# Kernel tuning notes

Measured on AMD Instinct MI355X. Metric: run time of the kernel, lower is better.

## Reference

```python
import jax, jax.numpy as jnp
import numpy as np

EPS = 1e-6
NEG_SLOPE = 0.2


def setup_inputs() -> dict:
    key = jax.random.key(0)
    k1, k2 = jax.random.split(key)
    B, D, T = 4, 512, 2048
    H, Dh = 8, 512 // 8
    x = jax.random.normal(k1, (B, D, T), dtype=jnp.float32)
    qkv = jax.random.normal(k2, (3, H, D, Dh), dtype=jnp.float32) * 0.02
    norm_w = jnp.ones((1,), dtype=jnp.float32)
    return {"x": x, "qkv": qkv, "norm_w": norm_w}


def reference(x, qkv, norm_w):
    B, D, T = x.shape
    H = qkv.shape[1]
    # leaky relu on channels-first input
    x = jnp.where(x >= 0, x, NEG_SLOPE * x)
    # fused QKV projection: (B,D,T),(3,H,D,Dh) -> (3,B,H,T,Dh)
    h = jnp.einsum('bdt,nhdD->nbhtD', x, qkv)
    # RMSNorm over the sequence axis (dim=-2), scalar learned weight
    denom = jnp.mean(h * h, axis=-2, keepdims=True)
    h = norm_w * (h / jnp.sqrt(denom + EPS))
    q, k, v = h[0], h[1], h[2]
    scale = jnp.sqrt(jnp.asarray(D // H, dtype=x.dtype))
    # manual attention: (B,H,T,T) score matrix
    attn = jax.nn.softmax(jnp.einsum('bhtD,bhTD->bhtT', q, k) / scale, axis=-1)
    # weighted values, output laid out (B,H,Dh,T) then merged to (B,D,T)
    out = jnp.einsum('bhtT,bhTD->bhDt', attn, v)
    return out.reshape(B, D, T)
```

## Files before the change

### kernel.cpp

```cpp
#include <hip/hip_runtime.h>
#include <cstddef>

#define B   4
#define D   512
#define T   2048
#define H   8
#define DH  64
#define NEG_SLOPE 0.2f
#define EPS 1e-6f
#define LOG2E 1.44269504088896340736f

typedef __attribute__((ext_vector_type(8))) short short8;
typedef __attribute__((ext_vector_type(4))) float float4v;

__device__ __forceinline__ float bf2f(ushort u) {
    unsigned int x = ((unsigned int)u) << 16;
    return __builtin_bit_cast(float, x);
}
__device__ __forceinline__ ushort f2bf(float f) {
    unsigned int x = __builtin_bit_cast(unsigned int, f);
    x = x + 0x7fffu + ((x >> 16) & 1u);
    return (ushort)(x >> 16);
}

__global__ __launch_bounds__(256) void transpose_lrelu(const float* __restrict__ src,
                                                       ushort* __restrict__ dst,
                                                       int src_ld, int dst_ld,
                                                       size_t src_mstride, size_t dst_mstride,
                                                       int do_lrelu,
                                                       float* __restrict__ zbuf, int zcount) {
    const int tid = threadIdx.x;
    if (zbuf != nullptr && blockIdx.x == 0 && blockIdx.y == 0 && blockIdx.z == 0) {
        for (int i = tid; i < zcount; i += 256) zbuf[i] = 0.f;
    }

    const int c0 = blockIdx.x * 64, r0 = blockIdx.y * 64;
    const float* s = src + blockIdx.z * src_mstride + (size_t)r0 * src_ld + c0;
    ushort*      d = dst + blockIdx.z * dst_mstride + (size_t)c0 * dst_ld + r0;

    __shared__ float Ls[64][68];

    const int rl = tid >> 4, c4 = (tid & 15) * 4;
    #pragma unroll
    for (int p = 0; p < 4; ++p) {
        float4 v = *(const float4*)(s + (size_t)(rl + p * 16) * src_ld + c4);
        if (do_lrelu) {
            v.x = fmaxf(v.x, NEG_SLOPE * v.x);
            v.y = fmaxf(v.y, NEG_SLOPE * v.y);
            v.z = fmaxf(v.z, NEG_SLOPE * v.z);
            v.w = fmaxf(v.w, NEG_SLOPE * v.w);
        }
        *(float4*)&Ls[rl + p * 16][c4] = v;
    }
    __syncthreads();

    const int tl = tid >> 2;
    #pragma unroll
    for (int it = 0; it < 2; ++it) {
        int ch = (tid & 3) + it * 4;
        ushort o[8];
        #pragma unroll
        for (int j = 0; j < 8; ++j) o[j] = f2bf(Ls[ch * 8 + j][tl]);
        *(uint4*)(d + (size_t)tl * dst_ld + ch * 8) = *(uint4*)o;
    }
}

__global__ __launch_bounds__(256) void qkv_mm(const ushort* __restrict__ xT,
                                              const ushort* __restrict__ WT,
                                              ushort* __restrict__ hb,
                                              ushort* __restrict__ vT,
                                              float* __restrict__ ssq) {
    const int tid = threadIdx.x, wave = tid >> 6, lane = tid & 63;
    const int quad = lane >> 4, l16 = lane & 15;
    const int wr = wave >> 1, wc = wave & 1;
    const int t0  = blockIdx.x * 128;
    const int gd0 = blockIdx.y * 128;
    const int b   = blockIdx.z;

    __shared__ ushort At[128 * 64];
    __shared__ ushort Bt[128 * 64];

    const ushort* xb = xT + (size_t)b * T * D + (size_t)t0 * D;
    const ushort* wb = WT + (size_t)gd0 * D;

    const int srow = lane >> 3;
    const int csrc = (lane & 7) ^ srow;

    float4v acc[4][4];
    #pragma unroll
    for (int i = 0; i < 4; ++i)
        #pragma unroll
        for (int j = 0; j < 4; ++j) acc[i][j] = (float4v){0.f, 0.f, 0.f, 0.f};

    for (int k0 = 0; k0 < D; k0 += 64) {
        #pragma unroll
        for (int i = 0; i < 4; ++i) {
            int rbase = wave * 32 + i * 8;
            int row = rbase + srow;
            const ushort* ga = xb + (size_t)row * D + k0 + csrc * 8;
            const ushort* gb = wb + (size_t)row * D + k0 + csrc * 8;
            __builtin_amdgcn_global_load_lds(
                (const __attribute__((address_space(1))) unsigned int*)ga,
                (__attribute__((address_space(3))) unsigned int*)&At[rbase * 64], 16, 0, 0);
            __builtin_amdgcn_global_load_lds(
                (const __attribute__((address_space(1))) unsigned int*)gb,
                (__attribute__((address_space(3))) unsigned int*)&Bt[rbase * 64], 16, 0, 0);
        }
        __syncthreads();

        #pragma unroll
        for (int kh = 0; kh < 2; ++kh) {
            short8 aF[4], bF[4];
            #pragma unroll
            for (int mt = 0; mt < 4; ++mt) {
                int row = wr * 64 + mt * 16 + l16;
                aF[mt] = *(const short8*)&At[row * 64 + (((kh * 4 + quad) ^ (l16 & 7)) * 8)];
            }
            #pragma unroll
            for (int nt = 0; nt < 4; ++nt) {
                int row = wc * 64 + nt * 16 + l16;
                bF[nt] = *(const short8*)&Bt[row * 64 + (((kh * 4 + quad) ^ (l16 & 7)) * 8)];
            }
            #pragma unroll
            for (int mt = 0; mt < 4; ++mt)
                #pragma unroll
                for (int nt = 0; nt < 4; ++nt)
                    acc[mt][nt] = __builtin_amdgcn_mfma_f32_16x16x32_bf16(
                        aF[mt], bF[nt], acc[mt][nt], 0, 0, 0);
        }
        __syncthreads();
    }

    const int g = blockIdx.y * 2 + wc;
    const int n = g >> 3, hh = g & 7;
    float colsq[4] = {0.f, 0.f, 0.f, 0.f};

    if (n < 2) {
        ushort* hbase = hb + (((size_t)n * B + b) * H + hh) * (size_t)T * DH;
        #pragma unroll
        for (int mt = 0; mt < 4; ++mt) {
            #pragma unroll
            for (int nt = 0; nt < 4; ++nt) {
                float4v c = acc[mt][nt];
                int dd = nt * 16 + l16;
                #pragma unroll
                for (int r = 0; r < 4; ++r) {
                    int t = t0 + wr * 64 + mt * 16 + quad * 4 + r;
                    hbase[(size_t)t * DH + dd] = f2bf(c[r]);
                    colsq[nt] += c[r] * c[r];
                }
            }
        }
    } else {
        ushort* vbase = vT + ((size_t)b * H + hh) * (size_t)DH * T;
        #pragma unroll
        for (int mt = 0; mt < 4; ++mt) {
            #pragma unroll
            for (int nt = 0; nt < 4; ++nt) {
                float4v c = acc[mt][nt];
                int dd = nt * 16 + l16;
                int t  = t0 + wr * 64 + mt * 16 + quad * 4;
                ushort4 pk;
                pk.x = f2bf(c[0]); pk.y = f2bf(c[1]);
                pk.z = f2bf(c[2]); pk.w = f2bf(c[3]);
                *(ushort4*)(vbase + (size_t)dd * T + t) = pk;
                colsq[nt] += c[0]*c[0] + c[1]*c[1] + c[2]*c[2] + c[3]*c[3];
            }
        }
    }
    #pragma unroll
    for (int nt = 0; nt < 4; ++nt) {
        float s = colsq[nt];
        s += __shfl_xor(s, 16);
        s += __shfl_xor(s, 32);
        if (quad == 0)
            atomicAdd(&ssq[(((size_t)n * B + b) * H + hh) * 64 + nt * 16 + l16], s);
    }
}

__global__ __launch_bounds__(256, 4) void flash_attn(const ushort* __restrict__ hb,
                                                     const ushort* __restrict__ vT,
                                                     const float* __restrict__ ssq,
                                                     const float* __restrict__ norm_w,
                                                     float* __restrict__ out) {
    const int tid  = threadIdx.x;
    const int wave = tid >> 6;
    const int lane = tid & 63;
    const int quad = lane >> 4;
    const int l16  = lane & 15;

    const int lin  = blockIdx.x;
    const int head = ((lin & 7) << 2) | ((lin >> 3) & 3);
    const int t0   = (lin >> 5) * 64;
    const int b    = head >> 3, hh = head & 7;

    const size_t slab = (size_t)B * H * T * DH;
    const ushort* qp = hb + (size_t)head * T * DH;
    const ushort* kp = hb + slab + (size_t)head * T * DH;
    const ushort* vp = vT + (size_t)head * DH * T;

    __shared__ ushort Kt[64 * 64];
    __shared__ ushort Vt[64 * 64];
    __shared__ ushort Pb[4][16 * 64];
    __shared__ float fqk[64], sv[64];

    if (tid < 64) {
        float nw = norm_w[0];
        float mq = ssq[(0 * B * H + head) * 64 + tid] * (1.0f / T) + EPS;
        float mk = ssq[(1 * B * H + head) * 64 + tid] * (1.0f / T) + EPS;
        float mv = ssq[(2 * B * H + head) * 64 + tid] * (1.0f / T) + EPS;
        fqk[tid] = nw * nw * rsqrtf(mq) * rsqrtf(mk) * 0.125f * LOG2E;
        sv[tid]  = nw * rsqrtf(mv);
    }
    __syncthreads();

    short8 bQ[2];
    {
        const ushort* qr = qp + (size_t)(t0 + wave * 16 + l16) * DH;
        #pragma unroll
        for (int kh = 0; kh < 2; ++kh) {
            short8 raw = *(const short8*)(qr + kh * 32 + quad * 8);
            #pragma unroll
            for (int j = 0; j < 8; ++j) {
                float f = bf2f((ushort)raw[j]) * fqk[kh * 32 + quad * 8 + j];
                bQ[kh][j] = (short)f2bf(f);
            }
        }
    }

    const int srow = lane >> 3;
    const int csrc = (lane & 7) ^ srow;
    const ushort* kA = kp + (size_t)(wave * 16 + srow) * DH + csrc * 8;
    const ushort* kB = kp + (size_t)(wave * 16 + 8 + srow) * DH + csrc * 8;
    const ushort* vA = vp + (size_t)(wave * 16 + srow) * T + csrc * 8;
    const ushort* vB = vp + (size_t)(wave * 16 + 8 + srow) * T + csrc * 8;

    float l_run = 0.f;
    float4v O[4];
    #pragma unroll
    for (int dt = 0; dt < 4; ++dt) O[dt] = (float4v){0.f, 0.f, 0.f, 0.f};

    for (int j0 = 0; j0 < T; j0 += 64) {
        __builtin_amdgcn_global_load_lds(
            (const __attribute__((address_space(1))) unsigned int*)(kA + (size_t)j0 * DH),
            (__attribute__((address_space(3))) unsigned int*)&Kt[(wave * 16) * 64], 16, 0, 0);
        __builtin_amdgcn_global_load_lds(
            (const __attribute__((address_space(1))) unsigned int*)(kB + (size_t)j0 * DH),
            (__attribute__((address_space(3))) unsigned int*)&Kt[(wave * 16 + 8) * 64], 16, 0, 0);
        __builtin_amdgcn_global_load_lds(
            (const __attribute__((address_space(1))) unsigned int*)(vA + j0),
            (__attribute__((address_space(3))) unsigned int*)&Vt[(wave * 16) * 64], 16, 0, 0);
        __builtin_amdgcn_global_load_lds(
            (const __attribute__((address_space(1))) unsigned int*)(vB + j0),
            (__attribute__((address_space(3))) unsigned int*)&Vt[(wave * 16 + 8) * 64], 16, 0, 0);
        __syncthreads();

        float4v S[4];
        #pragma unroll
        for (int mt = 0; mt < 4; ++mt) S[mt] = (float4v){0.f, 0.f, 0.f, 0.f};
        #pragma unroll
        for (int kh = 0; kh < 2; ++kh) {
            #pragma unroll
            for (int mt = 0; mt < 4; ++mt) {
                int row = mt * 16 + l16;
                short8 aK = *(const short8*)&Kt[row * 64 + (((kh * 4 + quad) ^ (l16 & 7)) * 8)];
                S[mt] = __builtin_amdgcn_mfma_f32_16x16x32_bf16(aK, bQ[kh], S[mt], 0, 0, 0);
            }
        }

        #pragma unroll
        for (int mt = 0; mt < 4; ++mt) {
            float p0 = __builtin_amdgcn_exp2f(S[mt][0]);
            float p1 = __builtin_amdgcn_exp2f(S[mt][1]);
            float p2 = __builtin_amdgcn_exp2f(S[mt][2]);
            float p3 = __builtin_amdgcn_exp2f(S[mt][3]);
            l_run += (p0 + p1) + (p2 + p3);
            unsigned int a0 = __builtin_bit_cast(unsigned int, p0) + 0x8000u;
            unsigned int a1 = __builtin_bit_cast(unsigned int, p1) + 0x8000u;
            unsigned int a2 = __builtin_bit_cast(unsigned int, p2) + 0x8000u;
            unsigned int a3 = __builtin_bit_cast(unsigned int, p3) + 0x8000u;
            uint2 pk;
            pk.x = __builtin_amdgcn_perm(a1, a0, 0x07060302u);
            pk.y = __builtin_amdgcn_perm(a3, a2, 0x07060302u);
            *(uint2*)&Pb[wave][l16 * 64 + (((mt * 2 + (quad >> 1)) ^ (l16 & 7)) * 8)
                               + (quad & 1) * 4] = pk;
        }

        #pragma unroll
        for (int kh = 0; kh < 2; ++kh) {
            short8 bP = *(const short8*)&Pb[wave][l16 * 64 + (((kh * 4 + quad) ^ (l16 & 7)) * 8)];
            #pragma unroll
            for (int dt = 0; dt < 4; ++dt) {
                int row = dt * 16 + l16;
                short8 aV = *(const short8*)&Vt[row * 64 + (((kh * 4 + quad) ^ (row & 7)) * 8)];
                O[dt] = __builtin_amdgcn_mfma_f32_16x16x32_bf16(aV, bP, O[dt], 0, 0, 0);
            }
        }
        __syncthreads();
    }

    float rs = l_run;
    rs += __shfl_xor(rs, 16);
    rs += __shfl_xor(rs, 32);
    float inv = 1.f / rs;
    const int t = t0 + wave * 16 + l16;
    #pragma unroll
    for (int dt = 0; dt < 4; ++dt) {
        #pragma unroll
        for (int r = 0; r < 4; ++r) {
            int dd = dt * 16 + quad * 4 + r;
            out[((size_t)b * D + hh * DH + dd) * T + t] = O[dt][r] * inv * sv[dd];
        }
    }
}

extern "C" void kernel_launch(void* const* d_in, const int* in_sizes, int n_in,
                              void* d_out, int out_size, void* d_ws, size_t ws_size,
                              hipStream_t stream) {
    const float* x      = (const float*)d_in[0];
    const float* qkv    = (const float*)d_in[1];
    const float* norm_w = (const float*)d_in[2];
    float* out = (float*)d_out;

    const size_t HB_BYTES = (size_t)2 * B * H * T * DH * 2;
    const size_t VT_BYTES = (size_t)B * H * DH * T * 2;
    const size_t XT_BYTES = (size_t)B * T * D * 2;
    const size_t WT_BYTES = (size_t)3 * H * DH * D * 2;
    ushort* hb  = (ushort*)d_ws;
    ushort* vT  = (ushort*)((char*)d_ws + HB_BYTES);
    ushort* xT  = (ushort*)((char*)d_ws + HB_BYTES + VT_BYTES);
    ushort* WT  = (ushort*)((char*)d_ws + HB_BYTES + VT_BYTES + XT_BYTES);
    float*  ssq = (float*)((char*)d_ws + HB_BYTES + VT_BYTES + XT_BYTES + WT_BYTES);
    const int SSQ_N = 3 * B * H * DH;

    transpose_lrelu<<<dim3(T / 64, D / 64, B), 256, 0, stream>>>(
        x, xT, T, D, (size_t)D * T, (size_t)T * D, 1, ssq, SSQ_N);
    transpose_lrelu<<<dim3(DH / 64, D / 64, 3 * H), 256, 0, stream>>>(
        qkv, WT, DH, D, (size_t)D * DH, (size_t)DH * D, 0, nullptr, 0);

    qkv_mm<<<dim3(T / 128, (3 * H * DH) / 128, B), 256, 0, stream>>>(xT, WT, hb, vT, ssq);
    flash_attn<<<dim3((T / 64) * B * H), 256, 0, stream>>>(hb, vT, ssq, norm_w, out);
}
```

Measured before the change: 155.0 us.

## Process two query groups per wave and load V fragments directly into registers

Each wave now handles 32 query rows (two 16-row groups), so the block covers 128 queries and every K tile staged in LDS and every V fragment is reused twice. V is no longer staged through LDS. Each lane reads its V MFMA operands straight from global memory into registers, which removes the Vt buffer and its LDS reads. The grid is halved and the launch bound drops to 2 blocks per CU to leave room for the doubled accumulators. The costs are more register pressure, fewer waves in flight, and uncoalesced-ish direct global V loads that the barrier no longer hides behind async LDS copies.

After: 173.1 us. 1.12x slower.

```diff
diff --git a/kernel.cpp b/kernel.cpp
--- a/kernel.cpp
+++ b/kernel.cpp
@@ -178,7 +178,7 @@
     }
 }
 
-__global__ __launch_bounds__(256, 4) void flash_attn(const ushort* __restrict__ hb,
+__global__ __launch_bounds__(256, 2) void flash_attn(const ushort* __restrict__ hb,
                                                      const ushort* __restrict__ vT,
                                                      const float* __restrict__ ssq,
                                                      const float* __restrict__ norm_w,
@@ -191,7 +191,7 @@
 
     const int lin  = blockIdx.x;
     const int head = ((lin & 7) << 2) | ((lin >> 3) & 3);
-    const int t0   = (lin >> 5) * 64;
+    const int t0   = (lin >> 5) * 128;
     const int b    = head >> 3, hh = head & 7;
 
     const size_t slab = (size_t)B * H * T * DH;
@@ -200,8 +200,7 @@
     const ushort* vp = vT + (size_t)head * DH * T;
 
     __shared__ ushort Kt[64 * 64];
-    __shared__ ushort Vt[64 * 64];
-    __shared__ ushort Pb[4][16 * 64];
+    __shared__ ushort Pb[4][2][16 * 64];
     __shared__ float fqk[64], sv[64];
 
     if (tid < 64) {
@@ -214,16 +213,17 @@
     }
     __syncthreads();
 
-    short8 bQ[2];
-    {
-        const ushort* qr = qp + (size_t)(t0 + wave * 16 + l16) * DH;
+    short8 bQ[2][2];
+    #pragma unroll
+    for (int g = 0; g < 2; ++g) {
+        const ushort* qr = qp + (size_t)(t0 + wave * 32 + g * 16 + l16) * DH;
         #pragma unroll
         for (int kh = 0; kh < 2; ++kh) {
             short8 raw = *(const short8*)(qr + kh * 32 + quad * 8);
             #pragma unroll
             for (int j = 0; j < 8; ++j) {
                 float f = bf2f((ushort)raw[j]) * fqk[kh * 32 + quad * 8 + j];
-                bQ[kh][j] = (short)f2bf(f);
+                bQ[g][kh][j] = (short)f2bf(f);
             }
         }
     }
@@ -232,13 +232,13 @@
     const int csrc = (lane & 7) ^ srow;
     const ushort* kA = kp + (size_t)(wave * 16 + srow) * DH + csrc * 8;
     const ushort* kB = kp + (size_t)(wave * 16 + 8 + srow) * DH + csrc * 8;
-    const ushort* vA = vp + (size_t)(wave * 16 + srow) * T + csrc * 8;
-    const ushort* vB = vp + (size_t)(wave * 16 + 8 + srow) * T + csrc * 8;
-
-    float l_run = 0.f;
-    float4v O[4];
-    #pragma unroll
-    for (int dt = 0; dt < 4; ++dt) O[dt] = (float4v){0.f, 0.f, 0.f, 0.f};
+
+    float l_run[2] = {0.f, 0.f};
+    float4v O[2][4];
+    #pragma unroll
+    for (int g = 0; g < 2; ++g)
+        #pragma unroll
+        for (int dt = 0; dt < 4; ++dt) O[g][dt] = (float4v){0.f, 0.f, 0.f, 0.f};
 
     for (int j0 = 0; j0 < T; j0 += 64) {
         __builtin_amdgcn_global_load_lds(
@@ -247,69 +247,88 @@
         __builtin_amdgcn_global_load_lds(
             (const __attribute__((address_space(1))) unsigned int*)(kB + (size_t)j0 * DH),
             (__attribute__((address_space(3))) unsigned int*)&Kt[(wave * 16 + 8) * 64], 16, 0, 0);
-        __builtin_amdgcn_global_load_lds(
-            (const __attribute__((address_space(1))) unsigned int*)(vA + j0),
-            (__attribute__((address_space(3))) unsigned int*)&Vt[(wave * 16) * 64], 16, 0, 0);
-        __builtin_amdgcn_global_load_lds(
-            (const __attribute__((address_space(1))) unsigned int*)(vB + j0),
-            (__attribute__((address_space(3))) unsigned int*)&Vt[(wave * 16 + 8) * 64], 16, 0, 0);
+
+        short8 aV[2][4];
+        #pragma unroll
+        for (int kh = 0; kh < 2; ++kh)
+            #pragma unroll
+            for (int dt = 0; dt < 4; ++dt)
+                aV[kh][dt] = *(const short8*)(vp + (size_t)(dt * 16 + l16) * T
+                                              + j0 + kh * 32 + quad * 8);
+
         __syncthreads();
 
-        float4v S[4];
-        #pragma unroll
-        for (int mt = 0; mt < 4; ++mt) S[mt] = (float4v){0.f, 0.f, 0.f, 0.f};
+        float4v S[2][4];
+        #pragma unroll
+        for (int g = 0; g < 2; ++g)
+            #pragma unroll
+            for (int mt = 0; mt < 4; ++mt) S[g][mt] = (float4v){0.f, 0.f, 0.f, 0.f};
         #pragma unroll
         for (int kh = 0; kh < 2; ++kh) {
+            short8 aK[4];
             #pragma unroll
             for (int mt = 0; mt < 4; ++mt) {
                 int row = mt * 16 + l16;
-                short8 aK = *(const short8*)&Kt[row * 64 + (((kh * 4 + quad) ^ (l16 & 7)) * 8)];
-                S[mt] = __builtin_amdgcn_mfma_f32_16x16x32_bf16(aK, bQ[kh], S[mt], 0, 0, 0);
-            }
-        }
-
-        #pragma unroll
-        for (int mt = 0; mt < 4; ++mt) {
-            float p0 = __builtin_amdgcn_exp2f(S[mt][0]);
-            float p1 = __builtin_amdgcn_exp2f(S[mt][1]);
-            float p2 = __builtin_amdgcn_exp2f(S[mt][2]);
-            float p3 = __builtin_amdgcn_exp2f(S[mt][3]);
-            l_run += (p0 + p1) + (p2 + p3);
-            unsigned int a0 = __builtin_bit_cast(unsigned int, p0) + 0x8000u;
-            unsigned int a1 = __builtin_bit_cast(unsigned int, p1) + 0x8000u;
-            unsigned int a2 = __builtin_bit_cast(unsigned int, p2) + 0x8000u;
-            unsigned int a3 = __builtin_bit_cast(unsigned int, p3) + 0x8000u;
-            uint2 pk;
-            pk.x = __builtin_amdgcn_perm(a1, a0, 0x07060302u);
-            pk.y = __builtin_amdgcn_perm(a3, a2, 0x07060302u);
-            *(uint2*)&Pb[wave][l16 * 64 + (((mt * 2 + (quad >> 1)) ^ (l16 & 7)) * 8)
-                               + (quad & 1) * 4] = pk;
-        }
-
-        #pragma unroll
-        for (int kh = 0; kh < 2; ++kh) {
-            short8 bP = *(const short8*)&Pb[wave][l16 * 64 + (((kh * 4 + quad) ^ (l16 & 7)) * 8)];
-            #pragma unroll
-            for (int dt = 0; dt < 4; ++dt) {
-                int row = dt * 16 + l16;
-                short8 aV = *(const short8*)&Vt[row * 64 + (((kh * 4 + quad) ^ (row & 7)) * 8)];
-                O[dt] = __builtin_amdgcn_mfma_f32_16x16x32_bf16(aV, bP, O[dt], 0, 0, 0);
-            }
-        }
+                aK[mt] = *(const short8*)&Kt[row * 64 + (((kh * 4 + quad) ^ (l16 & 7)) * 8)];
+            }
+            #pragma unroll
+            for (int g = 0; g < 2; ++g)
+                #pragma unroll
+                for (int mt = 0; mt < 4; ++mt)
+                    S[g][mt] = __builtin_amdgcn_mfma_f32_16x16x32_bf16(
+                        aK[mt], bQ[g][kh], S[g][mt], 0, 0, 0);
+        }
+
+        #pragma unroll
+        for (int g = 0; g < 2; ++g) {
+            #pragma unroll
+            for (int mt = 0; mt < 4; ++mt) {
+                float p0 = __builtin_amdgcn_exp2f(S[g][mt][0]);
+                float p1 = __builtin_amdgcn_exp2f(S[g][mt][1]);
+                float p2 = __builtin_amdgcn_exp2f(S[g][mt][2]);
+                float p3 = __builtin_amdgcn_exp2f(S[g][mt][3]);
+                l_run[g] += (p0 + p1) + (p2 + p3);
+                unsigned int a0 = __builtin_bit_cast(unsigned int, p0) + 0x8000u;
+                unsigned int a1 = __builtin_bit_cast(unsigned int, p1) + 0x8000u;
+                unsigned int a2 = __builtin_bit_cast(unsigned int, p2) + 0x8000u;
+                unsigned int a3 = __builtin_bit_cast(unsigned int, p3) + 0x8000u;
+                uint2 pk;
+                pk.x = __builtin_amdgcn_perm(a1, a0, 0x07060302u);
+                pk.y = __builtin_amdgcn_perm(a3, a2, 0x07060302u);
+                *(uint2*)&Pb[wave][g][l16 * 64 + (((mt * 2 + (quad >> 1)) ^ (l16 & 7)) * 8)
+                                      + (quad & 1) * 4] = pk;
+            }
+        }
+
+        #pragma unroll
+        for (int g = 0; g < 2; ++g) {
+            #pragma unroll
+            for (int kh = 0; kh < 2; ++kh) {
+                short8 bP = *(const short8*)&Pb[wave][g][l16 * 64 + (((kh * 4 + quad) ^ (l16 & 7)) * 8)];
+                #pragma unroll
+                for (int dt = 0; dt < 4; ++dt)
+                    O[g][dt] = __builtin_amdgcn_mfma_f32_16x16x32_bf16(
+                        aV[kh][dt], bP, O[g][dt], 0, 0, 0);
+            }
+        }
+
         __syncthreads();
     }
 
-    float rs = l_run;
-    rs += __shfl_xor(rs, 16);
-    rs += __shfl_xor(rs, 32);
-    float inv = 1.f / rs;
-    const int t = t0 + wave * 16 + l16;
-    #pragma unroll
-    for (int dt = 0; dt < 4; ++dt) {
-        #pragma unroll
-        for (int r = 0; r < 4; ++r) {
-            int dd = dt * 16 + quad * 4 + r;
-            out[((size_t)b * D + hh * DH + dd) * T + t] = O[dt][r] * inv * sv[dd];
+    #pragma unroll
+    for (int g = 0; g < 2; ++g) {
+        float rs = l_run[g];
+        rs += __shfl_xor(rs, 16);
+        rs += __shfl_xor(rs, 32);
+        float inv = 1.f / rs;
+        const int t = t0 + wave * 32 + g * 16 + l16;
+        #pragma unroll
+        for (int dt = 0; dt < 4; ++dt) {
+            #pragma unroll
+            for (int r = 0; r < 4; ++r) {
+                int dd = dt * 16 + quad * 4 + r;
+                out[((size_t)b * D + hh * DH + dd) * T + t] = O[g][dt][r] * inv * sv[dd];
+            }
         }
     }
 }
@@ -339,5 +358,5 @@
         qkv, WT, DH, D, (size_t)D * DH, (size_t)DH * D, 0, nullptr, 0);
 
     qkv_mm<<<dim3(T / 128, (3 * H * DH) / 128, B), 256, 0, stream>>>(xT, WT, hb, vT, ssq);
-    flash_attn<<<dim3((T / 64) * B * H), 256, 0, stream>>>(hb, vT, ssq, norm_w, out);
-}
+    flash_attn<<<dim3((T / 128) * B * H), 256, 0, stream>>>(hb, vT, ssq, norm_w, out);
+}
```
